# Kernel optimization log

Hardware: AMD Instinct MI355X
Metric: run time of the kernel (lower is better)

Reference implementation:

```python
import jax, jax.numpy as jnp
import numpy as np

B, N, H = 2048, 5, 5
IN, HID, OUT = 7, 2048, 512  # IN = 1 + c + c^2 with c = (H-1)//2 = 2


def setup_inputs() -> dict:
    key = jax.random.key(0)
    ks = jax.random.split(key, 7)
    k_in = 1.0 / np.sqrt(IN).astype(np.float32)
    k_h = 1.0 / np.sqrt(HID).astype(np.float32)
    return {
        "ins": jax.random.normal(ks[0], (B, N, H, H), jnp.float32),
        "w1": (jax.random.uniform(ks[1], (4, HID, IN), jnp.float32) - 0.5) * k_in,
        "b1": (jax.random.uniform(ks[2], (HID,), jnp.float32) - 0.5) * k_in,
        "w2": (jax.random.uniform(ks[3], (4, HID, HID), jnp.float32) - 0.5) * k_h,
        "b2": (jax.random.uniform(ks[4], (HID,), jnp.float32) - 0.5) * k_h,
        "w3": (jax.random.uniform(ks[5], (4, OUT, HID), jnp.float32) - 0.5) * k_h,
        "b3": (jax.random.uniform(ks[6], (OUT,), jnp.float32) - 0.5) * k_h,
        "ln_g": jnp.ones((HID,), jnp.float32),
        "ln_b": jnp.zeros((HID,), jnp.float32),
    }


def _rot90(x):
    # matches torch: x.flip(3).permute(0,1,3,2)
    return jnp.swapaxes(jnp.flip(x, axis=3), 2, 3)


def _orbit_stack(x):
    b, n = x.shape[0], x.shape[1]
    c = (x.shape[-1] - 1) // 2  # = 2 for H=5
    center = x[:, :, c, c]  # (B,N)
    parts = []
    xi = x
    for _ in range(4):  # fixed C4 group orbit, not a data loop
        parts.append(xi[:, :, :c, :c + 1].reshape(b, n, -1))  # (B,N,c+c^2)
        xi = _rot90(xi)
    orb = jnp.stack(parts, axis=-1)  # (B,N,c+c^2,4)
    cen = jnp.broadcast_to(center[..., None, None], (b, n, 1, 4))
    out = jnp.concatenate([cen, orb], axis=2)  # (B,N,n_orbits,4)
    return jnp.transpose(out, (0, 1, 3, 2))  # (B,N,4,n_orbits)


def _c4conv(w, bias, x):
    # block-circulant kernel: mat[g,h] = w[(h-g) % 4]
    mat = jnp.stack([jnp.roll(w, i, axis=0) for i in range(4)], axis=0)  # (4,4,out,in)
    return jnp.einsum('ghij,bnhj->bngi', mat, x) + bias


def _layernorm(x, g, b, eps=1e-5):
    m = jnp.mean(x, axis=-1, keepdims=True)
    v = jnp.mean(jnp.square(x - m), axis=-1, keepdims=True)
    return (x - m) / jnp.sqrt(v + eps) * g + b


def reference(ins, w1, b1, w2, b2, w3, b3, ln_g, ln_b):
    h = _orbit_stack(ins)                          # (B,N,4,7)
    h = jax.nn.relu(_c4conv(w1, b1, h))            # (B,N,4,HID)
    h = jax.nn.relu(_layernorm(_c4conv(w2, b2, h), ln_g, ln_b))
    return _c4conv(w3, b3, h)                      # (B,N,4,OUT)
```

## Files before the change

### kernel.cpp

```cpp
#include <hip/hip_runtime.h>
#include <stdint.h>


#define HID 2048
#define MROWS 10240

typedef float floatx4 __attribute__((ext_vector_type(4)));
typedef __bf16 bf16x8 __attribute__((ext_vector_type(8)));

__device__ __forceinline__ unsigned short f2bf(float f) {
  union { float f; unsigned int u; } v; v.f = f;
  unsigned int r = v.u + 0x7fffu + ((v.u >> 16) & 1u);
  return (unsigned short)(r >> 16);
}
__device__ __forceinline__ float bf2f(unsigned short s) {
  union { unsigned int u; float f; } v; v.u = ((unsigned int)s) << 16;
  return v.f;
}

template <int NO>
__global__ __launch_bounds__(256) void wtrans_kernel(const float* __restrict__ w,
                                                     unsigned short* __restrict__ W0s,
                                                     unsigned short* __restrict__ W2s,
                                                     unsigned short* __restrict__ Bc) {
  int idx = blockIdx.x * 256 + threadIdx.x;
  int i = idx >> 9, j4 = idx & 511;
  const float4* wp = (const float4*)w;
  float4 w0 = wp[0 * NO * 512 + i * 512 + j4];
  float4 w1 = wp[1 * NO * 512 + i * 512 + j4];
  float4 w2 = wp[2 * NO * 512 + i * 512 + j4];
  float4 w3 = wp[3 * NO * 512 + i * 512 + j4];
  ushort4 s0, s2, vr, vi, nvi;
#define DO(c)                                        \
  s0.c = f2bf(w0.c + w1.c + w2.c + w3.c);            \
  s2.c = f2bf(w0.c - w1.c + w2.c - w3.c);            \
  vr.c = f2bf(w0.c - w2.c);                          \
  vi.c = f2bf(w1.c - w3.c);                          \
  nvi.c = f2bf(-(w1.c - w3.c));
  DO(x) DO(y) DO(z) DO(w)
#undef DO
  ((ushort4*)W0s)[i * 512 + j4] = s0;
  ((ushort4*)W2s)[i * 512 + j4] = s2;
  ((ushort4*)Bc)[i * 1024 + j4] = vr;
  ((ushort4*)Bc)[i * 1024 + 512 + j4] = nvi;
  ((ushort4*)Bc)[(NO + i) * 1024 + j4] = vi;
  ((ushort4*)Bc)[(NO + i) * 1024 + 512 + j4] = vr;
}

__global__ __launch_bounds__(256) void layer1_kernel(const float* __restrict__ ins,
                                                     const float* __restrict__ w1,
                                                     const float* __restrict__ b1,
                                                     unsigned short* __restrict__ h1s,
                                                     int row0) {
  __shared__ float orbs[32][28];
  int t = threadIdx.x;
  int b0 = blockIdx.x * 32;
  int i = blockIdx.y * 256 + t;
  if (t < 32) {
    const float* x = ins + (size_t)(row0 + b0 + t) * 25;
    float v[25];
#pragma unroll
    for (int p = 0; p < 25; ++p) v[p] = x[p];
    float* o = orbs[t];
    o[0] = v[12]; o[7] = v[12]; o[14] = v[12]; o[21] = v[12];
#pragma unroll
    for (int r = 0; r < 2; ++r)
#pragma unroll
      for (int c = 0; c < 3; ++c) {
        int m = 1 + r * 3 + c;
        o[m]      = v[r * 5 + c];
        o[7 + m]  = v[c * 5 + (4 - r)];
        o[14 + m] = v[(4 - r) * 5 + (4 - c)];
        o[21 + m] = v[(4 - c) * 5 + r];
      }
  }
  __syncthreads();
  float w[4][7];
#pragma unroll
  for (int r = 0; r < 4; ++r)
#pragma unroll
    for (int j = 0; j < 7; ++j) w[r][j] = w1[(r * HID + i) * 7 + j];
  float bias = b1[i];
  for (int s = 0; s < 32; ++s) {
    float a[4] = {bias, bias, bias, bias};
#pragma unroll
    for (int hh = 0; hh < 4; ++hh)
#pragma unroll
      for (int j = 0; j < 7; ++j) {
        float ov = orbs[s][hh * 7 + j];
#pragma unroll
        for (int g = 0; g < 4; ++g) a[g] += w[(hh - g) & 3][j] * ov;
      }
    float h0 = fmaxf(a[0], 0.f), h1 = fmaxf(a[1], 0.f);
    float h2 = fmaxf(a[2], 0.f), h3 = fmaxf(a[3], 0.f);
    size_t base = (size_t)(b0 + s) * 8192 + i;
    h1s[base]        = f2bf(h0 + h1 + h2 + h3);
    h1s[base + 2048] = f2bf(h0 - h1 + h2 - h3);
    h1s[base + 4096] = f2bf(h0 - h2);
    h1s[base + 6144] = f2bf(h3 - h1);
  }
}

#define BM 128
#define BN 128
#define BK 64
#define PW 8

__global__ __launch_bounds__(256) void gemm_spec(const unsigned short* __restrict__ A,
                                                 const unsigned short* __restrict__ B0,
                                                 const unsigned short* __restrict__ B1,
                                                 const unsigned short* __restrict__ B2,
                                                 float* __restrict__ Cf,
                                                 unsigned short* __restrict__ Cb,
                                                 int s1, int s2, int N0, int ldc) {
  __shared__ __align__(16) unsigned short As[BM * BK];
  __shared__ __align__(16) unsigned short Bs[BN * BK];
  int tid = threadIdx.x;
  int wave = tid >> 6;
  int lane = tid & 63;
  int lane15 = lane & 15;
  int lane4 = lane >> 4;

  int flat = blockIdx.y * gridDim.x + blockIdx.x;
  int panel = flat / (PW * gridDim.y);
  int rem = flat % (PW * gridDim.y);
  int mt = rem / PW;
  int nt = panel * PW + rem % PW;
  int m0 = mt * BM;

  const unsigned short* Bp;
  int K, aoff, coff, nloc;
  if (nt < s1)      { Bp = B0; K = 2048; aoff = 0;    coff = 0;      nloc = nt * BN; }
  else if (nt < s2) { Bp = B1; K = 2048; aoff = 2048; coff = N0;     nloc = (nt - s1) * BN; }
  else              { Bp = B2; K = 4096; aoff = 4096; coff = 2 * N0; nloc = (nt - s2) * BN; }
  int ldb = K;

  int srow = wave * 8 + (lane >> 3);
  int scol = ((lane & 7) ^ (lane >> 3)) * 8;

  const unsigned short* Ag = A + (size_t)(m0 + srow) * 8192 + aoff + scol;
  const unsigned short* Bg = Bp + (size_t)(nloc + srow) * ldb + scol;

  int wm = (wave >> 1) * 64;
  int wn = (wave & 1) * 64;

  const floatx4 fz = {0.f, 0.f, 0.f, 0.f};
  floatx4 acc[4][4];
#pragma unroll
  for (int a = 0; a < 4; ++a)
#pragma unroll
    for (int b = 0; b < 4; ++b) acc[a][b] = fz;

  for (int k0 = 0; k0 < K; k0 += BK) {
#pragma unroll
    for (int q = 0; q < 4; ++q)
      __builtin_amdgcn_global_load_lds(
          (const __attribute__((address_space(1))) void*)(Ag + k0 + (size_t)q * 32 * 8192),
          (__attribute__((address_space(3))) void*)((char*)As + q * 4096 + wave * 1024),
          16, 0, 0);
#pragma unroll
    for (int q = 0; q < 4; ++q)
      __builtin_amdgcn_global_load_lds(
          (const __attribute__((address_space(1))) void*)(Bg + k0 + (size_t)q * 32 * ldb),
          (__attribute__((address_space(3))) void*)((char*)Bs + q * 4096 + wave * 1024),
          16, 0, 0);
    __syncthreads();
#pragma unroll
    for (int ks = 0; ks < 2; ++ks) {
      int chA = ((ks * 4 + lane4) ^ (lane15 & 7)) * 8;
      bf16x8 af[4], bfr[4];
#pragma unroll
      for (int mi = 0; mi < 4; ++mi)
        af[mi] = *(const bf16x8*)&As[(wm + mi * 16 + lane15) * BK + chA];
#pragma unroll
      for (int ni = 0; ni < 4; ++ni)
        bfr[ni] = *(const bf16x8*)&Bs[(wn + ni * 16 + lane15) * BK + chA];
#pragma unroll
      for (int mi = 0; mi < 4; ++mi)
#pragma unroll
        for (int ni = 0; ni < 4; ++ni)
          acc[mi][ni] = __builtin_amdgcn_mfma_f32_16x16x32_bf16(af[mi], bfr[ni], acc[mi][ni], 0, 0, 0);
    }
    __syncthreads();
  }

#pragma unroll
  for (int ni = 0; ni < 4; ++ni) {
    int col = coff + nloc + wn + ni * 16 + lane15;
#pragma unroll
    for (int mi = 0; mi < 4; ++mi) {
      int row = m0 + wm + mi * 16 + lane4 * 4;
      if (Cb) {
#pragma unroll
        for (int r = 0; r < 4; ++r)
          Cb[(size_t)(row + r) * ldc + col] = f2bf(acc[mi][ni][r]);
      } else {
#pragma unroll
        for (int r = 0; r < 4; ++r)
          Cf[(size_t)(row + r) * ldc + col] = acc[mi][ni][r];
      }
    }
  }
}

__global__ __launch_bounds__(256) void ln_spec_kernel(const unsigned short* __restrict__ C2,
                                                      const float* __restrict__ b2,
                                                      const float* __restrict__ ln_g,
                                                      const float* __restrict__ ln_b,
                                                      unsigned short* __restrict__ h1s) {
  int t = threadIdx.x;
  size_t base = (size_t)blockIdx.x * 8192;
  const ushort4* p = (const ushort4*)(C2 + base);
  const float4* bp2 = (const float4*)b2;
  float4 y[4][2];
  float s[4] = {0, 0, 0, 0}, q[4] = {0, 0, 0, 0};
#pragma unroll
  for (int hl = 0; hl < 2; ++hl) {
    int j = hl * 256 + t;
    ushort4 u0 = p[j], u2 = p[512 + j], ur = p[1024 + j], ui = p[1536 + j];
    float4 bb = bp2[j];
#define DO(c)                                                   \
  {                                                             \
    float v0 = bf2f(u0.c), v2 = bf2f(u2.c);                     \
    float vr = bf2f(ur.c), vi = bf2f(ui.c);                     \
    float e0 = 0.25f * (v0 + v2 + 2.f * vr) + bb.c;             \
    float e1 = 0.25f * (v0 - v2 - 2.f * vi) + bb.c;             \
    float e2 = 0.25f * (v0 + v2 - 2.f * vr) + bb.c;             \
    float e3 = 0.25f * (v0 - v2 + 2.f * vi) + bb.c;             \
    y[0][hl].c = e0; y[1][hl].c = e1; y[2][hl].c = e2; y[3][hl].c = e3; \
    s[0] += e0; q[0] += e0 * e0; s[1] += e1; q[1] += e1 * e1;   \
    s[2] += e2; q[2] += e2 * e2; s[3] += e3; q[3] += e3 * e3;   \
  }
    DO(x) DO(y) DO(z) DO(w)
#undef DO
  }
#pragma unroll
  for (int off = 32; off > 0; off >>= 1)
#pragma unroll
    for (int g = 0; g < 4; ++g) {
      s[g] += __shfl_down(s[g], off, 64);
      q[g] += __shfl_down(q[g], off, 64);
    }
  __shared__ float rs[4][4], rq[4][4];
  int w = t >> 6, l = t & 63;
  if (l == 0)
#pragma unroll
    for (int g = 0; g < 4; ++g) { rs[w][g] = s[g]; rq[w][g] = q[g]; }
  __syncthreads();
  float mean[4], rstd[4];
#pragma unroll
  for (int g = 0; g < 4; ++g) {
    float ss = rs[0][g] + rs[1][g] + rs[2][g] + rs[3][g];
    float qq = rq[0][g] + rq[1][g] + rq[2][g] + rq[3][g];
    mean[g] = ss * (1.f / HID);
    float var = qq * (1.f / HID) - mean[g] * mean[g];
    rstd[g] = rsqrtf(var + 1e-5f);
  }
  const float4* gp = (const float4*)ln_g;
  const float4* lbp = (const float4*)ln_b;
#pragma unroll
  for (int hl = 0; hl < 2; ++hl) {
    int j = hl * 256 + t;
    float4 gg = gp[j], lb = lbp[j];
    ushort4 o[4];
#define DO(c)                                                               \
  {                                                                         \
    float h0 = fmaxf((y[0][hl].c - mean[0]) * rstd[0] * gg.c + lb.c, 0.f);  \
    float h1 = fmaxf((y[1][hl].c - mean[1]) * rstd[1] * gg.c + lb.c, 0.f);  \
    float h2 = fmaxf((y[2][hl].c - mean[2]) * rstd[2] * gg.c + lb.c, 0.f);  \
    float h3 = fmaxf((y[3][hl].c - mean[3]) * rstd[3] * gg.c + lb.c, 0.f);  \
    o[0].c = f2bf(h0 + h1 + h2 + h3);                                       \
    o[1].c = f2bf(h0 - h1 + h2 - h3);                                       \
    o[2].c = f2bf(h0 - h2);                                                 \
    o[3].c = f2bf(h3 - h1);                                                 \
  }
    DO(x) DO(y) DO(z) DO(w)
#undef DO
    size_t ob = (size_t)blockIdx.x * 8192;
#pragma unroll
    for (int pl = 0; pl < 4; ++pl)
      ((ushort4*)(h1s + ob + pl * 2048))[j] = o[pl];
  }
}

__global__ __launch_bounds__(256) void out_ep_kernel(const float* __restrict__ Z,
                                                     const float* __restrict__ b3,
                                                     float* __restrict__ out) {
  int e = blockIdx.x * 256 + threadIdx.x;
  int row = e >> 9, i = e & 511;
  size_t base = (size_t)row * 2048;
  float z0 = Z[base + i], z2 = Z[base + 512 + i];
  float zr = Z[base + 1024 + i], zi = Z[base + 1536 + i];
  float bv = b3[i];
  out[base + i]        = 0.25f * (z0 + z2 + 2.f * zr) + bv;
  out[base + 512 + i]  = 0.25f * (z0 - z2 - 2.f * zi) + bv;
  out[base + 1024 + i] = 0.25f * (z0 + z2 - 2.f * zr) + bv;
  out[base + 1536 + i] = 0.25f * (z0 - z2 + 2.f * zi) + bv;
}

extern "C" void kernel_launch(void* const* d_in, const int* in_sizes, int n_in,
                              void* d_out, int out_size, void* d_ws, size_t ws_size,
                              hipStream_t stream) {
  const float* ins = (const float*)d_in[0];
  const float* w1  = (const float*)d_in[1];
  const float* b1  = (const float*)d_in[2];
  const float* w2  = (const float*)d_in[3];
  const float* b2  = (const float*)d_in[4];
  const float* w3  = (const float*)d_in[5];
  const float* b3  = (const float*)d_in[6];
  const float* lng = (const float*)d_in[7];
  const float* lnb = (const float*)d_in[8];
  float* out = (float*)d_out;
  char* ws = (char*)d_ws;

  unsigned short* W0s2 = (unsigned short*)ws;
  unsigned short* W2s2 = W0s2 + 4194304;
  unsigned short* Bc2  = W2s2 + 4194304;
  unsigned short* W0s3 = Bc2 + 16777216;
  unsigned short* W2s3 = W0s3 + 1048576;
  unsigned short* Bc3  = W2s3 + 1048576;
  const size_t WT_BYTES = 62914560ull;
  char* chunk_base = ws + WT_BYTES;

  static const int Pcand[10] = {1, 2, 4, 5, 8, 10, 16, 20, 40, 80};
  int P = 80;
  for (int pi = 0; pi < 10; ++pi) {
    size_t mc = (size_t)MROWS / Pcand[pi];
    size_t need = WT_BYTES + mc * 8192 * 2 * 2 + 256;
    if (need <= ws_size) { P = Pcand[pi]; break; }
  }
  const int Mc = MROWS / P;
  unsigned short* h1s = (unsigned short*)chunk_base;
  unsigned short* C2  = (unsigned short*)(chunk_base + (size_t)Mc * 8192 * 2);
  float*          Z   = (float*)C2;

  wtrans_kernel<2048><<<4096, 256, 0, stream>>>(w2, W0s2, W2s2, Bc2);
  wtrans_kernel<512><<<1024, 256, 0, stream>>>(w3, W0s3, W2s3, Bc3);

  for (int c = 0; c < P; ++c) {
    int row0 = c * Mc;
    layer1_kernel<<<dim3(Mc / 32, 8), 256, 0, stream>>>(ins, w1, b1, h1s, row0);
    gemm_spec<<<dim3(64, Mc / 128), 256, 0, stream>>>(h1s, W0s2, W2s2, Bc2, nullptr, C2,
                                                      16, 32, 2048, 8192);
    ln_spec_kernel<<<Mc, 256, 0, stream>>>(C2, b2, lng, lnb, h1s);
    gemm_spec<<<dim3(16, Mc / 128), 256, 0, stream>>>(h1s, W0s3, W2s3, Bc3, Z, nullptr,
                                                      4, 8, 512, 2048);
    out_ep_kernel<<<Mc * 2, 256, 0, stream>>>(Z, b3, out + (size_t)row0 * 2048);
  }
}
```

Baseline: 1.169 ms.

## Rewrite GEMM as 256x256 double-buffered 8-wave pipelined kernel with XCD swizzle

```diff
diff --git a/kernel.cpp b/kernel.cpp
--- a/kernel.cpp
+++ b/kernel.cpp
@@ -101,95 +101,153 @@
   }
 }
 
-#define BM 128
-#define BN 128
-#define BK 64
-#define PW 8
-
-__global__ __launch_bounds__(256) void gemm_spec(const unsigned short* __restrict__ A,
-                                                 const unsigned short* __restrict__ B0,
-                                                 const unsigned short* __restrict__ B1,
-                                                 const unsigned short* __restrict__ B2,
-                                                 float* __restrict__ Cf,
-                                                 unsigned short* __restrict__ Cb,
-                                                 int s1, int s2, int N0, int ldc) {
-  __shared__ __align__(16) unsigned short As[BM * BK];
-  __shared__ __align__(16) unsigned short Bs[BN * BK];
+#define PW 4
+
+
+__global__ __launch_bounds__(512, 2) void gemm_spec(const unsigned short* __restrict__ A,
+                                                    const unsigned short* __restrict__ B0,
+                                                    const unsigned short* __restrict__ B1,
+                                                    const unsigned short* __restrict__ B2,
+                                                    float* __restrict__ Cf,
+                                                    unsigned short* __restrict__ Cb,
+                                                    int s1, int s2, int N0, int ldc) {
+  __shared__ __align__(16) unsigned short As[2][16384];
+  __shared__ __align__(16) unsigned short Bs[2][16384];
   int tid = threadIdx.x;
-  int wave = tid >> 6;
-  int lane = tid & 63;
-  int lane15 = lane & 15;
-  int lane4 = lane >> 4;
-
+  int wave = tid >> 6, lane = tid & 63;
+  int lane15 = lane & 15, lane4 = lane >> 4, l7 = lane15 & 7;
+  int wm = wave >> 2, wn = wave & 3;
+  int wm64 = wm << 6, wn32 = wn << 5;
+
+  int nwg = gridDim.x * gridDim.y;
+  int q8 = nwg >> 3;
   int flat = blockIdx.y * gridDim.x + blockIdx.x;
-  int panel = flat / (PW * gridDim.y);
-  int rem = flat % (PW * gridDim.y);
+  int swz = (flat & 7) * q8 + (flat >> 3);
+  int pgy = PW * gridDim.y;
+  int panel = swz / pgy, rem = swz % pgy;
   int mt = rem / PW;
-  int nt = panel * PW + rem % PW;
-  int m0 = mt * BM;
+  int nt = panel * PW + (rem % PW);
+  int m0 = mt * 256;
 
   const unsigned short* Bp;
   int K, aoff, coff, nloc;
-  if (nt < s1)      { Bp = B0; K = 2048; aoff = 0;    coff = 0;      nloc = nt * BN; }
-  else if (nt < s2) { Bp = B1; K = 2048; aoff = 2048; coff = N0;     nloc = (nt - s1) * BN; }
-  else              { Bp = B2; K = 4096; aoff = 4096; coff = 2 * N0; nloc = (nt - s2) * BN; }
+  if (nt < s1)      { Bp = B0; K = 2048; aoff = 0;    coff = 0;      nloc = nt * 256; }
+  else if (nt < s2) { Bp = B1; K = 2048; aoff = 2048; coff = N0;     nloc = (nt - s1) * 256; }
+  else              { Bp = B2; K = 4096; aoff = 4096; coff = 2 * N0; nloc = (nt - s2) * 256; }
   int ldb = K;
 
-  int srow = wave * 8 + (lane >> 3);
-  int scol = ((lane & 7) ^ (lane >> 3)) * 8;
-
-  const unsigned short* Ag = A + (size_t)(m0 + srow) * 8192 + aoff + scol;
-  const unsigned short* Bg = Bp + (size_t)(nloc + srow) * ldb + scol;
-
-  int wm = (wave >> 1) * 64;
-  int wn = (wave & 1) * 64;
-
+  int srow = tid >> 3;
+  int scol = ((tid & 7) ^ ((tid >> 3) & 7)) << 3;
+  const unsigned short* Agb = A + (size_t)(m0 + srow) * 8192 + aoff + scol;
+  const unsigned short* Bgb = Bp + (size_t)(nloc + (srow & 31)) * ldb + scol;
+  int bs64 = (srow >> 5) << 6;
+
+#define STA(buf, mh, kk)                                                                              \
+  __builtin_amdgcn_global_load_lds(                                                                   \
+      (const __attribute__((address_space(1))) void*)(Agb + (size_t)((mh) * 64) * 8192 + (kk)),       \
+      (__attribute__((address_space(3))) void*)((char*)As[buf] + (mh) * 16384 + wave * 1024),         \
+      16, 0, 0);                                                                                      \
+  __builtin_amdgcn_global_load_lds(                                                                   \
+      (const __attribute__((address_space(1))) void*)(Agb + (size_t)((mh) * 64 + 128) * 8192 + (kk)), \
+      (__attribute__((address_space(3))) void*)((char*)As[buf] + (mh) * 16384 + 8192 + wave * 1024),  \
+      16, 0, 0)
+
+#define STB(buf, nh, kk)                                                                              \
+  __builtin_amdgcn_global_load_lds(                                                                   \
+      (const __attribute__((address_space(1))) void*)(Bgb + (size_t)(bs64 + (nh) * 32) * ldb + (kk)), \
+      (__attribute__((address_space(3))) void*)((char*)Bs[buf] + (nh) * 16384 + wave * 1024),         \
+      16, 0, 0);                                                                                      \
+  __builtin_amdgcn_global_load_lds(                                                                   \
+      (const __attribute__((address_space(1))) void*)(Bgb + (size_t)(bs64 + 128 + (nh) * 32) * ldb + (kk)), \
+      (__attribute__((address_space(3))) void*)((char*)Bs[buf] + (nh) * 16384 + 8192 + wave * 1024),  \
+      16, 0, 0)
+
+#define RAF(buf, mh)                                                                                  \
+  _Pragma("unroll") for (int mi_ = 0; mi_ < 4; ++mi_)                                                 \
+  _Pragma("unroll") for (int ks_ = 0; ks_ < 2; ++ks_)                                                 \
+      af[mi_][ks_] = *(const bf16x8*)((const char*)As[buf] +                                          \
+          (((mh) * 128 + wm64 + mi_ * 16 + lane15) << 7) + (((ks_ * 4 + lane4) ^ l7) << 4))
+
+#define RBF(dst, buf, nh)                                                                             \
+  _Pragma("unroll") for (int ni_ = 0; ni_ < 2; ++ni_)                                                 \
+  _Pragma("unroll") for (int ks_ = 0; ks_ < 2; ++ks_)                                                 \
+      dst[ni_][ks_] = *(const bf16x8*)((const char*)Bs[buf] +                                         \
+          (((nh) * 128 + wn32 + ni_ * 16 + lane15) << 7) + (((ks_ * 4 + lane4) ^ l7) << 4))
+
+#define MM(mh, nh, bF)                                                                                \
+  _Pragma("unroll") for (int mi_ = 0; mi_ < 4; ++mi_)                                                 \
+  _Pragma("unroll") for (int ni_ = 0; ni_ < 2; ++ni_)                                                 \
+  _Pragma("unroll") for (int ks_ = 0; ks_ < 2; ++ks_)                                                 \
+      acc[(mh) * 4 + mi_][(nh) * 2 + ni_] = __builtin_amdgcn_mfma_f32_16x16x32_bf16(                  \
+          af[mi_][ks_], bF[ni_][ks_], acc[(mh) * 4 + mi_][(nh) * 2 + ni_], 0, 0, 0)
+
+#define BAR() __builtin_amdgcn_s_barrier()
+#define LGKM0() asm volatile("s_waitcnt lgkmcnt(0)" ::: "memory")
+#define VM6() asm volatile("s_waitcnt vmcnt(6)" ::: "memory")
+
+  bf16x8 af[4][2], b0r[2][2], b1r[2][2];
   const floatx4 fz = {0.f, 0.f, 0.f, 0.f};
-  floatx4 acc[4][4];
-#pragma unroll
-  for (int a = 0; a < 4; ++a)
+  floatx4 acc[8][4];
+#pragma unroll
+  for (int a = 0; a < 8; ++a)
 #pragma unroll
     for (int b = 0; b < 4; ++b) acc[a][b] = fz;
 
-  for (int k0 = 0; k0 < K; k0 += BK) {
-#pragma unroll
-    for (int q = 0; q < 4; ++q)
-      __builtin_amdgcn_global_load_lds(
-          (const __attribute__((address_space(1))) void*)(Ag + k0 + (size_t)q * 32 * 8192),
-          (__attribute__((address_space(3))) void*)((char*)As + q * 4096 + wave * 1024),
-          16, 0, 0);
-#pragma unroll
-    for (int q = 0; q < 4; ++q)
-      __builtin_amdgcn_global_load_lds(
-          (const __attribute__((address_space(1))) void*)(Bg + k0 + (size_t)q * 32 * ldb),
-          (__attribute__((address_space(3))) void*)((char*)Bs + q * 4096 + wave * 1024),
-          16, 0, 0);
-    __syncthreads();
-#pragma unroll
-    for (int ks = 0; ks < 2; ++ks) {
-      int chA = ((ks * 4 + lane4) ^ (lane15 & 7)) * 8;
-      bf16x8 af[4], bfr[4];
-#pragma unroll
-      for (int mi = 0; mi < 4; ++mi)
-        af[mi] = *(const bf16x8*)&As[(wm + mi * 16 + lane15) * BK + chA];
-#pragma unroll
-      for (int ni = 0; ni < 4; ++ni)
-        bfr[ni] = *(const bf16x8*)&Bs[(wn + ni * 16 + lane15) * BK + chA];
-#pragma unroll
-      for (int mi = 0; mi < 4; ++mi)
-#pragma unroll
-        for (int ni = 0; ni < 4; ++ni)
-          acc[mi][ni] = __builtin_amdgcn_mfma_f32_16x16x32_bf16(af[mi], bfr[ni], acc[mi][ni], 0, 0, 0);
-    }
-    __syncthreads();
-  }
+  STA(0, 0, 0); STB(0, 0, 0); STB(0, 1, 0); STA(0, 1, 0);
+  STA(1, 0, 64); STB(1, 0, 64); STB(1, 1, 64);
+  VM6();
+  BAR();
+
+  for (int k0 = 0; k0 < K; k0 += 128) {
+    RAF(0, 0); RBF(b0r, 0, 0);
+    STA(1, 1, k0 + 64);
+    BAR(); LGKM0();
+    __builtin_amdgcn_s_setprio(1); MM(0, 0, b0r); __builtin_amdgcn_s_setprio(0);
+    BAR();
+    RBF(b1r, 0, 1);
+    STA(0, 0, k0 + 128);
+    BAR(); LGKM0();
+    __builtin_amdgcn_s_setprio(1); MM(0, 1, b1r); __builtin_amdgcn_s_setprio(0);
+    BAR();
+    RAF(0, 1);
+    STB(0, 0, k0 + 128);
+    BAR(); LGKM0();
+    __builtin_amdgcn_s_setprio(1); MM(1, 0, b0r); __builtin_amdgcn_s_setprio(0);
+    BAR();
+    STB(0, 1, k0 + 128);
+    BAR(); LGKM0();
+    __builtin_amdgcn_s_setprio(1); MM(1, 1, b1r); __builtin_amdgcn_s_setprio(0);
+    VM6();
+    BAR();
+    RAF(1, 0); RBF(b0r, 1, 0);
+    STA(0, 1, k0 + 128);
+    BAR(); LGKM0();
+    __builtin_amdgcn_s_setprio(1); MM(0, 0, b0r); __builtin_amdgcn_s_setprio(0);
+    BAR();
+    RBF(b1r, 1, 1);
+    STA(1, 0, k0 + 192);
+    BAR(); LGKM0();
+    __builtin_amdgcn_s_setprio(1); MM(0, 1, b1r); __builtin_amdgcn_s_setprio(0);
+    BAR();
+    RAF(1, 1);
+    STB(1, 0, k0 + 192);
+    BAR(); LGKM0();
+    __builtin_amdgcn_s_setprio(1); MM(1, 0, b0r); __builtin_amdgcn_s_setprio(0);
+    BAR();
+    STB(1, 1, k0 + 192);
+    BAR(); LGKM0();
+    __builtin_amdgcn_s_setprio(1); MM(1, 1, b1r); __builtin_amdgcn_s_setprio(0);
+    VM6();
+    BAR();
+  }
+  asm volatile("s_waitcnt vmcnt(0)" ::: "memory");
 
 #pragma unroll
   for (int ni = 0; ni < 4; ++ni) {
-    int col = coff + nloc + wn + ni * 16 + lane15;
-#pragma unroll
-    for (int mi = 0; mi < 4; ++mi) {
-      int row = m0 + wm + mi * 16 + lane4 * 4;
+    int col = coff + nloc + wn * 64 + (ni >> 1) * 32 + (ni & 1) * 16 + lane15;
+#pragma unroll
+    for (int mi = 0; mi < 8; ++mi) {
+      int row = m0 + wm * 128 + (mi >> 2) * 64 + (mi & 3) * 16 + lane4 * 4;
       if (Cb) {
 #pragma unroll
         for (int r = 0; r < 4; ++r)
@@ -201,6 +259,14 @@
       }
     }
   }
+#undef STA
+#undef STB
+#undef RAF
+#undef RBF
+#undef MM
+#undef BAR
+#undef LGKM0
+#undef VM6
 }
 
 __global__ __launch_bounds__(256) void ln_spec_kernel(const unsigned short* __restrict__ C2,
@@ -322,9 +388,9 @@
   const size_t WT_BYTES = 62914560ull;
   char* chunk_base = ws + WT_BYTES;
 
-  static const int Pcand[10] = {1, 2, 4, 5, 8, 10, 16, 20, 40, 80};
-  int P = 80;
-  for (int pi = 0; pi < 10; ++pi) {
+  static const int Pcand[8] = {1, 2, 4, 5, 8, 10, 20, 40};
+  int P = 40;
+  for (int pi = 0; pi < 8; ++pi) {
     size_t mc = (size_t)MROWS / Pcand[pi];
     size_t need = WT_BYTES + mc * 8192 * 2 * 2 + 256;
     if (need <= ws_size) { P = Pcand[pi]; break; }
@@ -340,11 +406,11 @@
   for (int c = 0; c < P; ++c) {
     int row0 = c * Mc;
     layer1_kernel<<<dim3(Mc / 32, 8), 256, 0, stream>>>(ins, w1, b1, h1s, row0);
-    gemm_spec<<<dim3(64, Mc / 128), 256, 0, stream>>>(h1s, W0s2, W2s2, Bc2, nullptr, C2,
-                                                      16, 32, 2048, 8192);
+    gemm_spec<<<dim3(32, Mc / 256), 512, 0, stream>>>(h1s, W0s2, W2s2, Bc2, nullptr, C2,
+                                                      8, 16, 2048, 8192);
     ln_spec_kernel<<<Mc, 256, 0, stream>>>(C2, b2, lng, lnb, h1s);
-    gemm_spec<<<dim3(16, Mc / 128), 256, 0, stream>>>(h1s, W0s3, W2s3, Bc3, Z, nullptr,
-                                                      4, 8, 512, 2048);
+    gemm_spec<<<dim3(8, Mc / 256), 512, 0, stream>>>(h1s, W0s3, W2s3, Bc3, Z, nullptr,
+                                                     2, 4, 512, 2048);
     out_ep_kernel<<<Mc * 2, 256, 0, stream>>>(Z, b3, out + (size_t)row0 * 2048);
   }
 }
```

After: 1.275 ms. 1.09x slower.
